# Kernel tuning notes

Measured on AMD Instinct MI355X. Metric: run time of the kernel, lower is better.

The kernel has to match this reference:

```python
import jax, jax.numpy as jnp
import numpy as np

WIN = 9
EPS = 1e-05


def _box_sum(x, win=WIN):
    # Separable 3D box-filter sum: mathematically identical to conv3d with a
    pad = win // 2
    for axis in range(3):  # spatial axes D, H, W
        kshape = [1, 1, 1]
        kshape[axis] = win
        filt = jnp.ones((1, 1, *kshape), dtype=x.dtype)  # OIDHW
        padding = [(pad, pad) if i == axis else (0, 0) for i in range(3)]
        x = jax.lax.conv_general_dilated(
            x, filt, window_strides=(1, 1, 1), padding=padding,
            dimension_numbers=('NCDHW', 'OIDHW', 'NCDHW'))
    return x


def setup_inputs() -> dict:
    key = jax.random.key(0)
    k1, k2 = jax.random.split(key)
    shape = (2, 1, 160, 192, 224)
    y_true = jax.random.uniform(k1, shape, dtype=jnp.float32)
    y_pred = jax.random.uniform(k2, shape, dtype=jnp.float32)
    return {"y_true": y_true, "y_pred": y_pred}


def reference(y_true, y_pred):
    ii, ji = y_true, y_pred
    win_size = jnp.asarray(float(WIN ** 3), dtype=ii.dtype)

    i_sum = _box_sum(ii)
    j_sum = _box_sum(ji)
    i2_sum = _box_sum(ii * ii)
    j2_sum = _box_sum(ji * ji)
    ij_sum = _box_sum(ii * ji)

    ui = i_sum / win_size
    uj = j_sum / win_size
    cross = ij_sum - uj * i_sum - ui * j_sum + ui * uj * win_size
    i_var = jnp.maximum(i2_sum - 2 * ui * i_sum + ui * ui * win_size, EPS)
    j_var = jnp.maximum(j2_sum - 2 * uj * j_sum + uj * uj * win_size, EPS)
    return -jnp.mean(cross * cross / (i_var * j_var))
```

## Files before the change

### kernel.cpp

```cpp
#include <hip/hip_runtime.h>

namespace {

constexpr int BD = 2;
constexpr int DD = 160, HH = 192, WW = 224;
constexpr float INV_WIN = 1.0f / 729.0f;
constexpr float EPSV = 1e-5f;

constexpr int TH = 16, TW = 16;
constexpr int DC = 80;
constexpr int NREAL = DC + 8;
constexpr int NPAIR = NREAL / 2;
constexpr int NCH = DD / DC;
constexpr int GX = WW / TW;
constexpr int GY = HH / TH;
constexpr int GZ = BD * NCH;
constexpr int NBLK = GX * GY * GZ;
constexpr int NXCD = 8;
constexpr int CPX = NBLK / NXCD;
constexpr double NTOT = (double)BD * DD * HH * WW;

constexpr int SR_FS = 452;
constexpr int SR_PL = 2280;
constexpr int SC_FS = 324;
constexpr int SC_PL = 1620;

}

__global__ __launch_bounds__(256)
void ncc_fused(const float* __restrict__ x, const float* __restrict__ y,
               float* __restrict__ bsum) {
  const int tid = threadIdx.x;

  const int lid = (int)blockIdx.x;
  const int nl  = (lid & (NXCD - 1)) * CPX + (lid >> 3);
  const int zb  = nl / (GX * GY);
  const int rem = nl - zb * (GX * GY);
  const int by  = rem / GX;
  const int bx  = rem - by * GX;

  const int w0 = bx * TW;
  const int h0 = by * TH;
  const int b  = zb / NCH;
  const int d0 = (zb - b * NCH) * DC;

  __shared__ __align__(16) float srowF[2][2 * SR_PL];
  __shared__ __align__(16) float scolF[2 * SC_PL];
  __shared__ float swsum[4];

  const bool s2a = tid < 192;
  const int p2  = tid / 96;
  const int t96 = tid - 96 * p2;
  const int r2  = t96 >> 2;
  const int seg = tid & 3;
  const int gh  = h0 - 4 + r2;
  const int gw0 = w0 - 4 + seg * 4;
  const bool hok = (unsigned)gh < (unsigned)HH;
  const bool fastw = (gw0 >= 0) && (gw0 + 11 < WW);
  const unsigned plane = (unsigned)HH * WW;

  auto prefetch = [&](int s, float4* vx, float4* vy) {
    const int din = d0 - 4 + s;
    const float4 z = make_float4(0.f, 0.f, 0.f, 0.f);
    vx[0] = vx[1] = vx[2] = z;
    vy[0] = vy[1] = vy[2] = z;
    if (s2a && hok && (s < NREAL) && (din >= 0) && (din < DD)) {
      const unsigned rb = ((unsigned)b * DD + (unsigned)din) * plane + (unsigned)gh * WW;
      if (fastw) {
        const float4* px = (const float4*)(x + rb + gw0);
        const float4* py = (const float4*)(y + rb + gw0);
        vx[0] = px[0]; vx[1] = px[1]; vx[2] = px[2];
        vy[0] = py[0]; vy[1] = py[1]; vy[2] = py[2];
      } else {
        float* fx = (float*)vx;
        float* fy = (float*)vy;
#pragma unroll
        for (int e = 0; e < 12; ++e) {
          const int gw = gw0 + e;
          if ((unsigned)gw < (unsigned)WW) {
            fx[e] = x[rb + gw];
            fy[e] = y[rb + gw];
          }
        }
      }
    }
  };

  const int t3  = tid - 96;
  const int p3  = t3 / 80;
  const int r3  = t3 - 80 * p3;
  const int f3  = r3 >> 4;
  const int wl3 = r3 & 15;

  const int ow = tid & 15;
  const int oh = tid >> 4;

  float rg0[9], rg1[9], rg2[9], rg3[9], rg4[9];
#pragma unroll
  for (int k = 0; k < 9; ++k) { rg0[k]=0.f; rg1[k]=0.f; rg2[k]=0.f; rg3[k]=0.f; rg4[k]=0.f; }
  float a0=0.f, a1=0.f, a2=0.f, a3=0.f, a4=0.f;
  float lsum = 0.0f;

  float4 px4[3], py4[3];
  prefetch(p2, px4, py4);

#pragma unroll 1
  for (int it = 0; it < (NPAIR + 1) / 9; ++it) {
#pragma unroll
    for (int u = 0; u < 9; ++u) {
      const int ss = 9 * it + u;

      float4 nx4[3], ny4[3];
      if (ss + 1 < NPAIR) prefetch(2 * (ss + 1) + p2, nx4, ny4);

      if (ss < NPAIR && s2a) {
        float xv[12], yv[12];
#pragma unroll
        for (int k = 0; k < 3; ++k) {
          *(float4*)&xv[4 * k] = px4[k];
          *(float4*)&yv[4 * k] = py4[k];
        }
        float s0=0.f, s1=0.f, s2=0.f, s3=0.f, s4=0.f;
#pragma unroll
        for (int k = 0; k < 9; ++k) {
          s0 += xv[k]; s1 += yv[k];
          s2 = fmaf(xv[k], xv[k], s2);
          s3 = fmaf(yv[k], yv[k], s3);
          s4 = fmaf(xv[k], yv[k], s4);
        }
        float* wb = &srowF[ss & 1][p2 * SR_PL + (seg * 4) * 28 + r2];
        wb[0 * SR_FS] = s0; wb[1 * SR_FS] = s1; wb[2 * SR_FS] = s2;
        wb[3 * SR_FS] = s3; wb[4 * SR_FS] = s4;
#pragma unroll
        for (int t = 1; t < 4; ++t) {
          const float xn = xv[8 + t], xo = xv[t - 1];
          const float yn = yv[8 + t], yo = yv[t - 1];
          s0 += xn - xo;
          s1 += yn - yo;
          s2 += fmaf(xn, xn, -(xo * xo));
          s3 += fmaf(yn, yn, -(yo * yo));
          s4 += fmaf(xn, yn, -(xo * yo));
          float* wt = wb + t * 28;
          wt[0 * SR_FS] = s0; wt[1 * SR_FS] = s1; wt[2 * SR_FS] = s2;
          wt[3 * SR_FS] = s3; wt[4 * SR_FS] = s4;
        }
      }

      if (ss >= 1 && tid >= 96) {
        const float* rp = &srowF[(ss - 1) & 1][p3 * SR_PL + f3 * SR_FS + wl3 * 28];
        float rv[24];
#pragma unroll
        for (int t = 0; t < 6; ++t) *(float4*)&rv[4 * t] = *(const float4*)&rp[4 * t];
        float acc = rv[0];
#pragma unroll
        for (int t = 1; t < 9; ++t) acc += rv[t];
        float ov[16];
        ov[0] = acc;
#pragma unroll
        for (int o = 1; o < 16; ++o) { acc += rv[o + 8] - rv[o - 1]; ov[o] = acc; }
        float* cp = &scolF[p3 * SC_PL + f3 * SC_FS + wl3 * 20];
#pragma unroll
        for (int t = 0; t < 4; ++t)
          *(float4*)&cp[4 * t] = make_float4(ov[4*t], ov[4*t+1], ov[4*t+2], ov[4*t+3]);
      }
      __syncthreads();

      if (ss >= 1) {
        const int sA  = 2 * (ss - 1);
        const int sB  = sA + 1;
        const int slA = (2 * u + 7) % 9;
        const int slB = (2 * u + 8) % 9;
        const float* cA = &scolF[ow * 20 + oh];
        const float* cB = cA + SC_PL;
        const float gA0 = cA[0*SC_FS], gA1 = cA[1*SC_FS], gA2 = cA[2*SC_FS],
                    gA3 = cA[3*SC_FS], gA4 = cA[4*SC_FS];
        const float gB0 = cB[0*SC_FS], gB1 = cB[1*SC_FS], gB2 = cB[2*SC_FS],
                    gB3 = cB[3*SC_FS], gB4 = cB[4*SC_FS];

        a0 += gA0 - rg0[slA]; rg0[slA] = gA0;
        a1 += gA1 - rg1[slA]; rg1[slA] = gA1;
        a2 += gA2 - rg2[slA]; rg2[slA] = gA2;
        a3 += gA3 - rg3[slA]; rg3[slA] = gA3;
        a4 += gA4 - rg4[slA]; rg4[slA] = gA4;
        if (sA >= 8) {
          const float cross = fmaf(-a0 * INV_WIN, a1, a4);
          const float iv = fmaxf(fmaf(-a0 * INV_WIN, a0, a2), EPSV);
          const float jv = fmaxf(fmaf(-a1 * INV_WIN, a1, a3), EPSV);
          lsum += (cross * cross) / (iv * jv);
        }
        a0 += gB0 - rg0[slB]; rg0[slB] = gB0;
        a1 += gB1 - rg1[slB]; rg1[slB] = gB1;
        a2 += gB2 - rg2[slB]; rg2[slB] = gB2;
        a3 += gB3 - rg3[slB]; rg3[slB] = gB3;
        a4 += gB4 - rg4[slB]; rg4[slB] = gB4;
        if (sB >= 8) {
          const float cross = fmaf(-a0 * INV_WIN, a1, a4);
          const float iv = fmaxf(fmaf(-a0 * INV_WIN, a0, a2), EPSV);
          const float jv = fmaxf(fmaf(-a1 * INV_WIN, a1, a3), EPSV);
          lsum += (cross * cross) / (iv * jv);
        }
      }
      __syncthreads();
      if (ss + 1 < NPAIR) {
#pragma unroll
        for (int k = 0; k < 3; ++k) { px4[k] = nx4[k]; py4[k] = ny4[k]; }
      }
    }
  }

#pragma unroll
  for (int off = 32; off > 0; off >>= 1) lsum += __shfl_down(lsum, off);
  if ((tid & 63) == 0) swsum[tid >> 6] = lsum;
  __syncthreads();
  if (tid == 0) bsum[nl] = swsum[0] + swsum[1] + swsum[2] + swsum[3];
}

__global__ __launch_bounds__(256)
void ncc_finalize(const float* __restrict__ bsum, float* __restrict__ out) {
  double s = 0.0;
  for (int i = threadIdx.x; i < NBLK; i += 256) s += (double)bsum[i];
#pragma unroll
  for (int off = 32; off > 0; off >>= 1) s += __shfl_down(s, off);
  __shared__ double sh[4];
  if ((threadIdx.x & 63) == 0) sh[threadIdx.x >> 6] = s;
  __syncthreads();
  if (threadIdx.x == 0)
    out[0] = (float)(-(sh[0] + sh[1] + sh[2] + sh[3]) / NTOT);
}

extern "C" void kernel_launch(void* const* d_in, const int* in_sizes, int n_in,
                              void* d_out, int out_size, void* d_ws, size_t ws_size,
                              hipStream_t stream) {
  const float* x = (const float*)d_in[0];
  const float* y = (const float*)d_in[1];
  float* bsum = (float*)d_ws;
  float* out  = (float*)d_out;

  ncc_fused<<<dim3(NBLK), dim3(256), 0, stream>>>(x, y, bsum);
  ncc_finalize<<<1, dim3(256), 0, stream>>>(bsum, out);
}
```

Measured before the change: 214.2 us.

## Retile NCC kernel to 32x16 tiles, shallow depth chunks and 512 threads

Changes the block tile from 16x16 by 80 depth slices to 32x16 by 16 depth slices, giving about 2.5x as many blocks. Each block now runs 512 threads, and the row and column shared-memory layouts are re-padded for the taller tile. The depth loop is now fully unrolled and the 9-slot ring index is computed directly. The intent is more parallelism and better latency hiding, but the 8-slice depth halo is now re-read for every 16 slices, so redundant global loads and stencil work increase.

```diff
diff --git a/kernel.cpp b/kernel.cpp
--- a/kernel.cpp
+++ b/kernel.cpp
@@ -7,8 +7,8 @@
 constexpr float INV_WIN = 1.0f / 729.0f;
 constexpr float EPSV = 1e-5f;
 
-constexpr int TH = 16, TW = 16;
-constexpr int DC = 80;
+constexpr int TH = 32, TW = 16;
+constexpr int DC = 16;
 constexpr int NREAL = DC + 8;
 constexpr int NPAIR = NREAL / 2;
 constexpr int NCH = DD / DC;
@@ -18,16 +18,19 @@
 constexpr int NBLK = GX * GY * GZ;
 constexpr int NXCD = 8;
 constexpr int CPX = NBLK / NXCD;
+constexpr int IR = TH + 8;
 constexpr double NTOT = (double)BD * DD * HH * WW;
 
-constexpr int SR_FS = 452;
-constexpr int SR_PL = 2280;
-constexpr int SC_FS = 324;
-constexpr int SC_PL = 1620;
-
-}
-
-__global__ __launch_bounds__(256)
+constexpr int ROWP  = 44;
+constexpr int SR_FS = 708;
+constexpr int SR_PL = 3560;
+constexpr int OHP   = 36;
+constexpr int SC_FS = 580;
+constexpr int SC_PL = 2900;
+
+}
+
+__global__ __launch_bounds__(512)
 void ncc_fused(const float* __restrict__ x, const float* __restrict__ y,
                float* __restrict__ bsum) {
   const int tid = threadIdx.x;
@@ -46,12 +49,12 @@
 
   __shared__ __align__(16) float srowF[2][2 * SR_PL];
   __shared__ __align__(16) float scolF[2 * SC_PL];
-  __shared__ float swsum[4];
-
-  const bool s2a = tid < 192;
-  const int p2  = tid / 96;
-  const int t96 = tid - 96 * p2;
-  const int r2  = t96 >> 2;
+  __shared__ float swsum[8];
+
+  const bool s2a = tid < 320;
+  const int p2  = tid / 160;
+  const int t160 = tid - 160 * p2;
+  const int r2  = t160 >> 2;
   const int seg = tid & 3;
   const int gh  = h0 - 4 + r2;
   const int gw0 = w0 - 4 + seg * 4;
@@ -86,7 +89,8 @@
     }
   };
 
-  const int t3  = tid - 96;
+  const bool s3a = (tid >= 320) && (tid < 480);
+  const int t3  = tid - 320;
   const int p3  = t3 / 80;
   const int r3  = t3 - 80 * p3;
   const int f3  = r3 >> 4;
@@ -104,53 +108,53 @@
   float4 px4[3], py4[3];
   prefetch(p2, px4, py4);
 
-#pragma unroll 1
-  for (int it = 0; it < (NPAIR + 1) / 9; ++it) {
-#pragma unroll
-    for (int u = 0; u < 9; ++u) {
-      const int ss = 9 * it + u;
-
-      float4 nx4[3], ny4[3];
-      if (ss + 1 < NPAIR) prefetch(2 * (ss + 1) + p2, nx4, ny4);
-
-      if (ss < NPAIR && s2a) {
-        float xv[12], yv[12];
-#pragma unroll
-        for (int k = 0; k < 3; ++k) {
-          *(float4*)&xv[4 * k] = px4[k];
-          *(float4*)&yv[4 * k] = py4[k];
-        }
-        float s0=0.f, s1=0.f, s2=0.f, s3=0.f, s4=0.f;
-#pragma unroll
-        for (int k = 0; k < 9; ++k) {
-          s0 += xv[k]; s1 += yv[k];
-          s2 = fmaf(xv[k], xv[k], s2);
-          s3 = fmaf(yv[k], yv[k], s3);
-          s4 = fmaf(xv[k], yv[k], s4);
-        }
-        float* wb = &srowF[ss & 1][p2 * SR_PL + (seg * 4) * 28 + r2];
-        wb[0 * SR_FS] = s0; wb[1 * SR_FS] = s1; wb[2 * SR_FS] = s2;
-        wb[3 * SR_FS] = s3; wb[4 * SR_FS] = s4;
-#pragma unroll
-        for (int t = 1; t < 4; ++t) {
-          const float xn = xv[8 + t], xo = xv[t - 1];
-          const float yn = yv[8 + t], yo = yv[t - 1];
-          s0 += xn - xo;
-          s1 += yn - yo;
-          s2 += fmaf(xn, xn, -(xo * xo));
-          s3 += fmaf(yn, yn, -(yo * yo));
-          s4 += fmaf(xn, yn, -(xo * yo));
-          float* wt = wb + t * 28;
-          wt[0 * SR_FS] = s0; wt[1 * SR_FS] = s1; wt[2 * SR_FS] = s2;
-          wt[3 * SR_FS] = s3; wt[4 * SR_FS] = s4;
-        }
-      }
-
-      if (ss >= 1 && tid >= 96) {
-        const float* rp = &srowF[(ss - 1) & 1][p3 * SR_PL + f3 * SR_FS + wl3 * 28];
+#pragma unroll
+  for (int ss = 0; ss <= NPAIR; ++ss) {
+    float4 nx4[3], ny4[3];
+    if (ss + 1 < NPAIR) prefetch(2 * (ss + 1) + p2, nx4, ny4);
+
+    if (ss < NPAIR && s2a) {
+      float xv[12], yv[12];
+#pragma unroll
+      for (int k = 0; k < 3; ++k) {
+        *(float4*)&xv[4 * k] = px4[k];
+        *(float4*)&yv[4 * k] = py4[k];
+      }
+      float s0=0.f, s1=0.f, s2=0.f, s3=0.f, s4=0.f;
+#pragma unroll
+      for (int k = 0; k < 9; ++k) {
+        s0 += xv[k]; s1 += yv[k];
+        s2 = fmaf(xv[k], xv[k], s2);
+        s3 = fmaf(yv[k], yv[k], s3);
+        s4 = fmaf(xv[k], yv[k], s4);
+      }
+      float* wb = &srowF[ss & 1][p2 * SR_PL + (seg * 4) * ROWP + r2];
+      wb[0 * SR_FS] = s0; wb[1 * SR_FS] = s1; wb[2 * SR_FS] = s2;
+      wb[3 * SR_FS] = s3; wb[4 * SR_FS] = s4;
+#pragma unroll
+      for (int t = 1; t < 4; ++t) {
+        const float xn = xv[8 + t], xo = xv[t - 1];
+        const float yn = yv[8 + t], yo = yv[t - 1];
+        s0 += xn - xo;
+        s1 += yn - yo;
+        s2 += fmaf(xn, xn, -(xo * xo));
+        s3 += fmaf(yn, yn, -(yo * yo));
+        s4 += fmaf(xn, yn, -(xo * yo));
+        float* wt = wb + t * ROWP;
+        wt[0 * SR_FS] = s0; wt[1 * SR_FS] = s1; wt[2 * SR_FS] = s2;
+        wt[3 * SR_FS] = s3; wt[4 * SR_FS] = s4;
+      }
+    }
+
+    if (ss >= 1 && s3a) {
+      const float* rp = &srowF[(ss - 1) & 1][p3 * SR_PL + f3 * SR_FS + wl3 * ROWP];
+      float* cp = &scolF[p3 * SC_PL + f3 * SC_FS + wl3 * OHP];
+#pragma unroll
+      for (int hf = 0; hf < 2; ++hf) {
+        const float* rph = rp + 16 * hf;
         float rv[24];
 #pragma unroll
-        for (int t = 0; t < 6; ++t) *(float4*)&rv[4 * t] = *(const float4*)&rp[4 * t];
+        for (int t = 0; t < 6; ++t) *(float4*)&rv[4 * t] = *(const float4*)&rph[4 * t];
         float acc = rv[0];
 #pragma unroll
         for (int t = 1; t < 9; ++t) acc += rv[t];
@@ -158,53 +162,53 @@
         ov[0] = acc;
 #pragma unroll
         for (int o = 1; o < 16; ++o) { acc += rv[o + 8] - rv[o - 1]; ov[o] = acc; }
-        float* cp = &scolF[p3 * SC_PL + f3 * SC_FS + wl3 * 20];
+        float* cph = cp + 16 * hf;
 #pragma unroll
         for (int t = 0; t < 4; ++t)
-          *(float4*)&cp[4 * t] = make_float4(ov[4*t], ov[4*t+1], ov[4*t+2], ov[4*t+3]);
-      }
-      __syncthreads();
-
-      if (ss >= 1) {
-        const int sA  = 2 * (ss - 1);
-        const int sB  = sA + 1;
-        const int slA = (2 * u + 7) % 9;
-        const int slB = (2 * u + 8) % 9;
-        const float* cA = &scolF[ow * 20 + oh];
-        const float* cB = cA + SC_PL;
-        const float gA0 = cA[0*SC_FS], gA1 = cA[1*SC_FS], gA2 = cA[2*SC_FS],
-                    gA3 = cA[3*SC_FS], gA4 = cA[4*SC_FS];
-        const float gB0 = cB[0*SC_FS], gB1 = cB[1*SC_FS], gB2 = cB[2*SC_FS],
-                    gB3 = cB[3*SC_FS], gB4 = cB[4*SC_FS];
-
-        a0 += gA0 - rg0[slA]; rg0[slA] = gA0;
-        a1 += gA1 - rg1[slA]; rg1[slA] = gA1;
-        a2 += gA2 - rg2[slA]; rg2[slA] = gA2;
-        a3 += gA3 - rg3[slA]; rg3[slA] = gA3;
-        a4 += gA4 - rg4[slA]; rg4[slA] = gA4;
-        if (sA >= 8) {
-          const float cross = fmaf(-a0 * INV_WIN, a1, a4);
-          const float iv = fmaxf(fmaf(-a0 * INV_WIN, a0, a2), EPSV);
-          const float jv = fmaxf(fmaf(-a1 * INV_WIN, a1, a3), EPSV);
-          lsum += (cross * cross) / (iv * jv);
-        }
-        a0 += gB0 - rg0[slB]; rg0[slB] = gB0;
-        a1 += gB1 - rg1[slB]; rg1[slB] = gB1;
-        a2 += gB2 - rg2[slB]; rg2[slB] = gB2;
-        a3 += gB3 - rg3[slB]; rg3[slB] = gB3;
-        a4 += gB4 - rg4[slB]; rg4[slB] = gB4;
-        if (sB >= 8) {
-          const float cross = fmaf(-a0 * INV_WIN, a1, a4);
-          const float iv = fmaxf(fmaf(-a0 * INV_WIN, a0, a2), EPSV);
-          const float jv = fmaxf(fmaf(-a1 * INV_WIN, a1, a3), EPSV);
-          lsum += (cross * cross) / (iv * jv);
-        }
-      }
-      __syncthreads();
-      if (ss + 1 < NPAIR) {
-#pragma unroll
-        for (int k = 0; k < 3; ++k) { px4[k] = nx4[k]; py4[k] = ny4[k]; }
-      }
+          *(float4*)&cph[4 * t] = make_float4(ov[4*t], ov[4*t+1], ov[4*t+2], ov[4*t+3]);
+      }
+    }
+    __syncthreads();
+
+    if (ss >= 1) {
+      const int sA  = 2 * (ss - 1);
+      const int sB  = sA + 1;
+      const int slA = sA % 9;
+      const int slB = sB % 9;
+      const float* cA = &scolF[ow * OHP + oh];
+      const float* cB = cA + SC_PL;
+      const float gA0 = cA[0*SC_FS], gA1 = cA[1*SC_FS], gA2 = cA[2*SC_FS],
+                  gA3 = cA[3*SC_FS], gA4 = cA[4*SC_FS];
+      const float gB0 = cB[0*SC_FS], gB1 = cB[1*SC_FS], gB2 = cB[2*SC_FS],
+                  gB3 = cB[3*SC_FS], gB4 = cB[4*SC_FS];
+
+      a0 += gA0 - rg0[slA]; rg0[slA] = gA0;
+      a1 += gA1 - rg1[slA]; rg1[slA] = gA1;
+      a2 += gA2 - rg2[slA]; rg2[slA] = gA2;
+      a3 += gA3 - rg3[slA]; rg3[slA] = gA3;
+      a4 += gA4 - rg4[slA]; rg4[slA] = gA4;
+      if (sA >= 8) {
+        const float cross = fmaf(-a0 * INV_WIN, a1, a4);
+        const float iv = fmaxf(fmaf(-a0 * INV_WIN, a0, a2), EPSV);
+        const float jv = fmaxf(fmaf(-a1 * INV_WIN, a1, a3), EPSV);
+        lsum += (cross * cross) / (iv * jv);
+      }
+      a0 += gB0 - rg0[slB]; rg0[slB] = gB0;
+      a1 += gB1 - rg1[slB]; rg1[slB] = gB1;
+      a2 += gB2 - rg2[slB]; rg2[slB] = gB2;
+      a3 += gB3 - rg3[slB]; rg3[slB] = gB3;
+      a4 += gB4 - rg4[slB]; rg4[slB] = gB4;
+      if (sB >= 8) {
+        const float cross = fmaf(-a0 * INV_WIN, a1, a4);
+        const float iv = fmaxf(fmaf(-a0 * INV_WIN, a0, a2), EPSV);
+        const float jv = fmaxf(fmaf(-a1 * INV_WIN, a1, a3), EPSV);
+        lsum += (cross * cross) / (iv * jv);
+      }
+    }
+    __syncthreads();
+    if (ss + 1 < NPAIR) {
+#pragma unroll
+      for (int k = 0; k < 3; ++k) { px4[k] = nx4[k]; py4[k] = ny4[k]; }
     }
   }
 
@@ -212,7 +216,12 @@
   for (int off = 32; off > 0; off >>= 1) lsum += __shfl_down(lsum, off);
   if ((tid & 63) == 0) swsum[tid >> 6] = lsum;
   __syncthreads();
-  if (tid == 0) bsum[nl] = swsum[0] + swsum[1] + swsum[2] + swsum[3];
+  if (tid == 0) {
+    float s = 0.f;
+#pragma unroll
+    for (int k = 0; k < 8; ++k) s += swsum[k];
+    bsum[nl] = s;
+  }
 }
 
 __global__ __launch_bounds__(256)
@@ -236,6 +245,6 @@
   float* bsum = (float*)d_ws;
   float* out  = (float*)d_out;
 
-  ncc_fused<<<dim3(NBLK), dim3(256), 0, stream>>>(x, y, bsum);
+  ncc_fused<<<dim3(NBLK), dim3(512), 0, stream>>>(x, y, bsum);
   ncc_finalize<<<1, dim3(256), 0, stream>>>(bsum, out);
 }
```

Measured after the change: 222.0 us. +3.6%, slower.
